# Performance work log

Measured on AMD Instinct MI355X. Metric: run time of the kernel, lower is better.

Reference implementation:

```python
import jax, jax.numpy as jnp
import numpy as np

IN_FEATURES = 4096
OUT_FEATURES = 11008
GROUPSIZE = 128
N_GROUPS = IN_FEATURES // GROUPSIZE  # 32


def setup_inputs() -> dict:
    key = jax.random.key(0)
    k1, k2, k3 = jax.random.split(key, 3)
    inp = jax.random.normal(k1, (2, 2048, IN_FEATURES), dtype=jnp.float32)
    # int8 quantized weights stored as int8
    weight = jax.random.randint(k2, (OUT_FEATURES, IN_FEATURES), -128, 128, dtype=jnp.int32).astype(jnp.int8)
    # per-(output-channel, group) positive scales
    scales = jax.random.uniform(k3, (OUT_FEATURES, N_GROUPS), dtype=jnp.float32) * 0.01 + 1e-4
    return {"input": inp, "weight": weight, "scales": scales}


def reference(input, weight, scales):
    # Dequantize: w[o, g, j] = int8_w[o, g, j] * scales[o, g]
    O, I = weight.shape
    w = weight.astype(input.dtype).reshape(O, N_GROUPS, GROUPSIZE)
    w = (w * scales[:, :, None].astype(input.dtype)).reshape(O, I)
    # F.linear: input @ w.T  -> [B, S, O]
    return jnp.einsum("bsi,oi->bso", input, w)
```

## Files before the change

kernel.cpp:

```cpp
#include <hip/hip_runtime.h>

#define MDIM 4096
#define KDIM 4096
#define NDIM 11008
#define NGROUPS 32

#define BM 256
#define BN 256
#define BK 64
#define NT (KDIM / BK)
#define KB (KDIM * 2)

typedef _Float16 f16x8 __attribute__((ext_vector_type(8)));
typedef float f32x4 __attribute__((ext_vector_type(4)));

typedef const unsigned int __attribute__((address_space(1))) *gas_t;
typedef unsigned int __attribute__((address_space(3))) *las_t;

__device__ __forceinline__ void gld_lds16(const void *g, void *l) {
  __builtin_amdgcn_global_load_lds((gas_t)g, (las_t)l, 16, 0, 0);
}

#define BAR() asm volatile("s_barrier" ::: "memory")
#define VMW4() asm volatile("s_waitcnt vmcnt(4)" ::: "memory")
#define VMW0() asm volatile("s_waitcnt vmcnt(0)" ::: "memory")
#define FENCE() __builtin_amdgcn_sched_barrier(0)

__global__ __launch_bounds__(256) void cvt_a_kernel(const float *__restrict__ a,
                                                    _Float16 *__restrict__ o) {
  const int n8 = (MDIM * KDIM) / 8;
  for (int i = blockIdx.x * blockDim.x + threadIdx.x; i < n8;
       i += gridDim.x * blockDim.x) {
    const float4 v0 = *(const float4 *)(a + (size_t)i * 8);
    const float4 v1 = *(const float4 *)(a + (size_t)i * 8 + 4);
    f16x8 h;
    h[0] = (_Float16)v0.x; h[1] = (_Float16)v0.y;
    h[2] = (_Float16)v0.z; h[3] = (_Float16)v0.w;
    h[4] = (_Float16)v1.x; h[5] = (_Float16)v1.y;
    h[6] = (_Float16)v1.z; h[7] = (_Float16)v1.w;
    *(f16x8 *)(o + (size_t)i * 8) = h;
  }
}

__global__ __launch_bounds__(256) void cvt_w_kernel(const int *__restrict__ w,
                                                    const float *__restrict__ s,
                                                    _Float16 *__restrict__ o) {
  const int n8 = (NDIM * KDIM) / 8;
  for (int i = blockIdx.x * blockDim.x + threadIdx.x; i < n8;
       i += gridDim.x * blockDim.x) {
    const size_t base = (size_t)i * 8;
    const int row = (int)(base >> 12);
    const int g = ((int)(base & (KDIM - 1))) >> 7;
    const float sc = s[row * NGROUPS + g];
    const int4 w0 = *(const int4 *)(w + base);
    const int4 w1 = *(const int4 *)(w + base + 4);
    f16x8 h;
    h[0] = (_Float16)((float)w0.x * sc); h[1] = (_Float16)((float)w0.y * sc);
    h[2] = (_Float16)((float)w0.z * sc); h[3] = (_Float16)((float)w0.w * sc);
    h[4] = (_Float16)((float)w1.x * sc); h[5] = (_Float16)((float)w1.y * sc);
    h[6] = (_Float16)((float)w1.z * sc); h[7] = (_Float16)((float)w1.w * sc);
    *(f16x8 *)(o + base) = h;
  }
}

__global__ __launch_bounds__(512, 2) void gemm_8phase(
    const _Float16 *__restrict__ Ah, const _Float16 *__restrict__ Wh,
    float *__restrict__ C) {
  __shared__ __align__(16) char Sh[163840];

  const int tid = threadIdx.x;
  const int l = tid & 63;
  const int w = tid >> 6;
  const int wm = w >> 2;
  const int wn = w & 3;

  const int wg = blockIdx.x;
  const int swz = (wg & 7) * 86 + (wg >> 3);
  const int bx = swz / 16;
  const int by = swz % 16;

  const int srow = l >> 3;
  const int gk = ((l & 7) ^ srow) * 16;
  const char *Ag =
      (const char *)Ah + (size_t)(by * BM + w * 8 + srow) * KB + gk;
  const char *Bg =
      (const char *)Wh + (size_t)(bx * BN + w * 8 + srow) * KB + gk;

  const int laneRow = (l & 15) * (BK * 2);
  const int kx0 = ((l >> 4) * 16) ^ ((l & 7) * 16);
  const int kx1 = kx0 ^ 64;

  f32x4 acc[8][4] = {};
  f16x8 af0[4][2], af1[4][2], bf0[2][2], bf1[2][2];

  unsigned aC = 0, aN = 32768;
  unsigned bC = 65536, bN = 98304, bS = 131072;

#define STAGE2_A(KT, OFF, S0)                                                 \
  {                                                                           \
    const char *ap_ = Ag + (size_t)(KT) * (BK * 2);                           \
    gld_lds16(ap_ + (size_t)(S0) * (64 * KB),                                 \
              (void *)(Sh + (OFF) + (S0) * 8192 + w * 1024));                 \
    gld_lds16(ap_ + (size_t)((S0) + 1) * (64 * KB),                           \
              (void *)(Sh + (OFF) + ((S0) + 1) * 8192 + w * 1024));           \
  }

#define STAGE2_B(KT, OFF, S0)                                                 \
  {                                                                           \
    const char *bp_ = Bg + (size_t)(KT) * (BK * 2);                           \
    gld_lds16(bp_ + (size_t)(S0) * (64 * KB),                                 \
              (void *)(Sh + (OFF) + (S0) * 8192 + w * 1024));                 \
    gld_lds16(bp_ + (size_t)((S0) + 1) * (64 * KB),                           \
              (void *)(Sh + (OFF) + ((S0) + 1) * 8192 + w * 1024));           \
  }

#define LDA_Q(DST, QM, BASE)                                                  \
  {                                                                           \
    const char *ba_ = (BASE) + (wm * 128 + (QM) * 64) * (BK * 2) + laneRow;   \
    _Pragma("unroll") for (int mi = 0; mi < 4; ++mi) {                        \
      DST[mi][0] = *(const f16x8 *)(ba_ + mi * 2048 + kx0);                   \
      DST[mi][1] = *(const f16x8 *)(ba_ + mi * 2048 + kx1);                   \
    }                                                                         \
  }

#define LDB_Q(DST, QN, BASE)                                                  \
  {                                                                           \
    const char *bb_ = (BASE) + (wn * 64 + (QN) * 32) * (BK * 2) + laneRow;    \
    _Pragma("unroll") for (int nj = 0; nj < 2; ++nj) {                        \
      DST[nj][0] = *(const f16x8 *)(bb_ + nj * 2048 + kx0);                   \
      DST[nj][1] = *(const f16x8 *)(bb_ + nj * 2048 + kx1);                   \
    }                                                                         \
  }

#define MMA_Q(AF, BF, QM, QN)                                                 \
  __builtin_amdgcn_s_setprio(1);                                              \
  _Pragma("unroll") for (int ks = 0; ks < 2; ++ks)                            \
      _Pragma("unroll") for (int mi = 0; mi < 4; ++mi)                        \
          _Pragma("unroll") for (int nj = 0; nj < 2; ++nj)                    \
              acc[(QM) * 4 + mi][(QN) * 2 + nj] =                             \
                  __builtin_amdgcn_mfma_f32_16x16x32_f16(                     \
                      AF[mi][ks], BF[nj][ks],                                 \
                      acc[(QM) * 4 + mi][(QN) * 2 + nj], 0, 0, 0);            \
  __builtin_amdgcn_s_setprio(0);

  STAGE2_A(0, aC, 0); STAGE2_A(0, aC, 2);
  STAGE2_B(0, bC, 0); STAGE2_B(0, bC, 2);
  STAGE2_B(1, bN, 0); STAGE2_B(1, bN, 2);
  VMW4();
  BAR();
  LDA_Q(af0, 0, (const char *)Sh + aC);
  LDB_Q(bf0, 0, (const char *)Sh + bC);

#pragma unroll 2
  for (int t = 0; t < NT; ++t) {
    const bool s1 = (t + 1 < NT);
    const bool s2 = (t + 2 < NT);
    const char *Ac = (const char *)Sh + aC;
    const char *An = (const char *)Sh + aN;
    const char *Bc = (const char *)Sh + bC;
    const char *Bn = (const char *)Sh + bN;

    if (s1) { STAGE2_A(t + 1, aN, 0); STAGE2_A(t + 1, aN, 2); }
    if (s2) { STAGE2_B(t + 2, bS, 0); STAGE2_B(t + 2, bS, 2); }

    LDB_Q(bf1, 1, Bc);
    FENCE();
    MMA_Q(af0, bf0, 0, 0);

    LDA_Q(af1, 1, Ac);
    FENCE();
    MMA_Q(af0, bf1, 0, 1);

    MMA_Q(af1, bf1, 1, 1);
    MMA_Q(af1, bf0, 1, 0);

    if (s2) { VMW4(); } else { VMW0(); }
    BAR();
    if (s1) {
      LDA_Q(af0, 0, An);
      LDB_Q(bf0, 0, Bn);
    }

    { const unsigned ta = aC; aC = aN; aN = ta; }
    { const unsigned tb = bC; bC = bN; bN = bS; bS = tb; }
  }

#undef STAGE2_A
#undef STAGE2_B
#undef LDA_Q
#undef LDB_Q
#undef MMA_Q

  const int fr = l & 15, fq = l >> 4;
  float *Cb = C + (size_t)(by * BM + wm * 128) * NDIM + bx * BN + wn * 64;
#pragma unroll
  for (int i = 0; i < 8; ++i)
#pragma unroll
    for (int j = 0; j < 4; ++j)
#pragma unroll
      for (int r = 0; r < 4; ++r)
        Cb[(size_t)(i * 16 + fq * 4 + r) * NDIM + j * 16 + fr] = acc[i][j][r];
}

__global__ __launch_bounds__(256) void gemm_fused(const float *__restrict__ A,
                                                  const int *__restrict__ W,
                                                  const float *__restrict__ S,
                                                  float *__restrict__ C) {
  __shared__ _Float16 Asf[128 * 64];
  __shared__ _Float16 Bsf[128 * 64];
  const int tid = threadIdx.x;
  const int lane = tid & 63;
  const int wv = tid >> 6;
  const int wm = wv >> 1, wn = wv & 1;
  const int bx = blockIdx.x, by = blockIdx.y;
  const int srow = tid >> 1;
  const int skof = (tid & 1) * 32;

  const float *Ab = A + (size_t)(by * 128 + srow) * KDIM + skof;
  const int *Wb = W + (size_t)(bx * 128 + srow) * KDIM + skof;
  const float *Sb = S + (size_t)(bx * 128 + srow) * NGROUPS;

  f32x4 acc[4][4] = {};
  float4 ar[8];
  int4 wr[8];
  float sc;

#pragma unroll
  for (int u = 0; u < 8; ++u) {
    ar[u] = *(const float4 *)(Ab + u * 4);
    wr[u] = *(const int4 *)(Wb + u * 4);
  }
  sc = Sb[0];

  const int fr = lane & 15;
  const int fq = lane >> 4;
  const int kbase = fq * 8;

  for (int kt = 0; kt < KDIM / 64; ++kt) {
    __syncthreads();
    _Float16 *Ad = &Asf[srow * 64 + skof];
    _Float16 *Bd = &Bsf[srow * 64 + skof];
#pragma unroll
    for (int u = 0; u < 4; ++u) {
      const float4 a0 = ar[2 * u], a1 = ar[2 * u + 1];
      const int4 b0 = wr[2 * u], b1 = wr[2 * u + 1];
      f16x8 ha, hb;
      ha[0] = (_Float16)a0.x; ha[1] = (_Float16)a0.y;
      ha[2] = (_Float16)a0.z; ha[3] = (_Float16)a0.w;
      ha[4] = (_Float16)a1.x; ha[5] = (_Float16)a1.y;
      ha[6] = (_Float16)a1.z; ha[7] = (_Float16)a1.w;
      hb[0] = (_Float16)((float)b0.x * sc); hb[1] = (_Float16)((float)b0.y * sc);
      hb[2] = (_Float16)((float)b0.z * sc); hb[3] = (_Float16)((float)b0.w * sc);
      hb[4] = (_Float16)((float)b1.x * sc); hb[5] = (_Float16)((float)b1.y * sc);
      hb[6] = (_Float16)((float)b1.z * sc); hb[7] = (_Float16)((float)b1.w * sc);
      *(f16x8 *)(Ad + u * 8) = ha;
      *(f16x8 *)(Bd + u * 8) = hb;
    }
    if (kt + 1 < KDIM / 64) {
      const float *An = Ab + (kt + 1) * 64;
      const int *Wn = Wb + (kt + 1) * 64;
#pragma unroll
      for (int u = 0; u < 8; ++u) {
        ar[u] = *(const float4 *)(An + u * 4);
        wr[u] = *(const int4 *)(Wn + u * 4);
      }
      sc = Sb[(kt + 1) >> 1];
    }
    __syncthreads();
#pragma unroll
    for (int ks = 0; ks < 2; ++ks) {
      f16x8 afv[4], bfv[4];
      const int kof = ks * 32 + kbase;
#pragma unroll
      for (int i = 0; i < 4; ++i) {
        afv[i] = *(const f16x8 *)&Asf[(wm * 64 + i * 16 + fr) * 64 + kof];
        bfv[i] = *(const f16x8 *)&Bsf[(wn * 64 + i * 16 + fr) * 64 + kof];
      }
#pragma unroll
      for (int i = 0; i < 4; ++i)
#pragma unroll
        for (int j = 0; j < 4; ++j)
          acc[i][j] = __builtin_amdgcn_mfma_f32_16x16x32_f16(afv[i], bfv[j],
                                                             acc[i][j], 0, 0, 0);
    }
  }

  float *Cb = C + (size_t)(by * 128 + wm * 64) * NDIM + bx * 128 + wn * 64;
#pragma unroll
  for (int i = 0; i < 4; ++i)
#pragma unroll
    for (int j = 0; j < 4; ++j)
#pragma unroll
      for (int r = 0; r < 4; ++r)
        Cb[(size_t)(i * 16 + fq * 4 + r) * NDIM + j * 16 + fr] = acc[i][j][r];
}

extern "C" void kernel_launch(void *const *d_in, const int *in_sizes, int n_in,
                              void *d_out, int out_size, void *d_ws,
                              size_t ws_size, hipStream_t stream) {
  (void)in_sizes; (void)n_in; (void)out_size;
  const float *A = (const float *)d_in[0];
  const int *W = (const int *)d_in[1];
  const float *S = (const float *)d_in[2];
  float *C = (float *)d_out;

  const size_t needA = (size_t)MDIM * KDIM * sizeof(_Float16);
  const size_t needW = (size_t)NDIM * KDIM * sizeof(_Float16);

  if (ws_size >= needA + needW) {
    _Float16 *Ahp = (_Float16 *)d_ws;
    _Float16 *Whp = (_Float16 *)((char *)d_ws + needA);
    cvt_a_kernel<<<2048, 256, 0, stream>>>(A, Ahp);
    cvt_w_kernel<<<2048, 256, 0, stream>>>(W, S, Whp);
    gemm_8phase<<<(MDIM / BM) * (NDIM / BN), 512, 0, stream>>>(Ahp, Whp, C);
  } else {
    dim3 grid(NDIM / 128, MDIM / 128);
    gemm_fused<<<grid, 256, 0, stream>>>(A, W, S, C);
  }
}
```

Baseline: 409.1 us.

## Interleave LDS fragment reads with MFMA chunks and ping-pong B registers

Splits the per-quarter LDS fragment loads and MFMA blocks into smaller pieces and interleaves them, so shared-memory reads are spread between MFMA groups. The last quarter's MFMAs now run after the barrier and overlap the loads of the next tile's A and B fragments. B fragment registers alternate between two buffers across a manually unrolled pair of tiles. The aim is to hide LDS latency and barrier stalls behind matrix work. The cost is more live registers, which may pressure occupancy, and heavier reliance on the compiler keeping the intended order across the fences.

```diff
diff --git a/kernel.cpp b/kernel.cpp
--- a/kernel.cpp
+++ b/kernel.cpp
@@ -91,7 +91,7 @@
   const int kx1 = kx0 ^ 64;
 
   f32x4 acc[8][4] = {};
-  f16x8 af0[4][2], af1[4][2], bf0[2][2], bf1[2][2];
+  f16x8 af0[4][2], af1[4][2], bfA[2][2], bfB[2][2];
 
   unsigned aC = 0, aN = 32768;
   unsigned bC = 65536, bN = 98304, bS = 131072;
@@ -114,81 +114,102 @@
               (void *)(Sh + (OFF) + ((S0) + 1) * 8192 + w * 1024));           \
   }
 
-#define LDA_Q(DST, QM, BASE)                                                  \
+#define RDA2(DST, MI, QM, BASE)                                               \
   {                                                                           \
     const char *ba_ = (BASE) + (wm * 128 + (QM) * 64) * (BK * 2) + laneRow;   \
-    _Pragma("unroll") for (int mi = 0; mi < 4; ++mi) {                        \
-      DST[mi][0] = *(const f16x8 *)(ba_ + mi * 2048 + kx0);                   \
-      DST[mi][1] = *(const f16x8 *)(ba_ + mi * 2048 + kx1);                   \
-    }                                                                         \
-  }
-
-#define LDB_Q(DST, QN, BASE)                                                  \
+    DST[MI][0] = *(const f16x8 *)(ba_ + (MI) * 2048 + kx0);                   \
+    DST[MI][1] = *(const f16x8 *)(ba_ + (MI) * 2048 + kx1);                   \
+  }
+
+#define RDB2(DST, NJ, QN, BASE)                                               \
   {                                                                           \
     const char *bb_ = (BASE) + (wn * 64 + (QN) * 32) * (BK * 2) + laneRow;    \
-    _Pragma("unroll") for (int nj = 0; nj < 2; ++nj) {                        \
-      DST[nj][0] = *(const f16x8 *)(bb_ + nj * 2048 + kx0);                   \
-      DST[nj][1] = *(const f16x8 *)(bb_ + nj * 2048 + kx1);                   \
-    }                                                                         \
-  }
+    DST[NJ][0] = *(const f16x8 *)(bb_ + (NJ) * 2048 + kx0);                   \
+    DST[NJ][1] = *(const f16x8 *)(bb_ + (NJ) * 2048 + kx1);                   \
+  }
+
+#define MMA4(AF, BF, QM, QN, KS, MI0)                                         \
+  __builtin_amdgcn_s_setprio(1);                                              \
+  _Pragma("unroll") for (int mi = (MI0); mi < (MI0) + 2; ++mi)                \
+      _Pragma("unroll") for (int nj = 0; nj < 2; ++nj)                        \
+          acc[(QM) * 4 + mi][(QN) * 2 + nj] =                                 \
+              __builtin_amdgcn_mfma_f32_16x16x32_f16(                         \
+                  AF[mi][KS], BF[nj][KS],                                     \
+                  acc[(QM) * 4 + mi][(QN) * 2 + nj], 0, 0, 0);                \
+  __builtin_amdgcn_s_setprio(0);
 
 #define MMA_Q(AF, BF, QM, QN)                                                 \
-  __builtin_amdgcn_s_setprio(1);                                              \
-  _Pragma("unroll") for (int ks = 0; ks < 2; ++ks)                            \
-      _Pragma("unroll") for (int mi = 0; mi < 4; ++mi)                        \
-          _Pragma("unroll") for (int nj = 0; nj < 2; ++nj)                    \
-              acc[(QM) * 4 + mi][(QN) * 2 + nj] =                             \
-                  __builtin_amdgcn_mfma_f32_16x16x32_f16(                     \
-                      AF[mi][ks], BF[nj][ks],                                 \
-                      acc[(QM) * 4 + mi][(QN) * 2 + nj], 0, 0, 0);            \
-  __builtin_amdgcn_s_setprio(0);
+  MMA4(AF, BF, QM, QN, 0, 0); MMA4(AF, BF, QM, QN, 0, 2);                     \
+  MMA4(AF, BF, QM, QN, 1, 0); MMA4(AF, BF, QM, QN, 1, 2);
+
+#define TILE(T, B0, B1)                                                       \
+  {                                                                           \
+    const bool s1 = (T) + 1 < NT;                                             \
+    const bool s2 = (T) + 2 < NT;                                             \
+    const char *Ac = (const char *)Sh + aC;                                   \
+    const char *An = (const char *)Sh + aN;                                   \
+    const char *Bc = (const char *)Sh + bC;                                   \
+    const char *Bn = (const char *)Sh + bN;                                   \
+       \
+    if (s1) { STAGE2_A((T) + 1, aN, 0); STAGE2_A((T) + 1, aN, 2); }           \
+    if (s2) { STAGE2_B((T) + 2, bS, 0); STAGE2_B((T) + 2, bS, 2); }           \
+                 \
+    RDB2(B1, 0, 1, Bc);                                                       \
+    FENCE(); MMA4(af0, B0, 0, 0, 0, 0);                                       \
+    RDB2(B1, 1, 1, Bc);                                                       \
+    FENCE(); MMA4(af0, B0, 0, 0, 0, 2);                                       \
+    FENCE(); MMA4(af0, B0, 0, 0, 1, 0);                                       \
+    FENCE(); MMA4(af0, B0, 0, 0, 1, 2);                                       \
+                \
+    RDA2(af1, 0, 1, Ac); RDA2(af1, 1, 1, Ac);                                 \
+    FENCE(); MMA4(af0, B1, 0, 1, 0, 0);                                       \
+    RDA2(af1, 2, 1, Ac); RDA2(af1, 3, 1, Ac);                                 \
+    FENCE(); MMA4(af0, B1, 0, 1, 0, 2);                                       \
+    FENCE(); MMA4(af0, B1, 0, 1, 1, 0);                                       \
+    FENCE(); MMA4(af0, B1, 0, 1, 1, 2);                                       \
+                                           \
+    MMA_Q(af1, B1, 1, 1);                                                     \
+              \
+    if (s2) { VMW4(); } else { VMW0(); }                                      \
+    BAR();                                                                    \
+             \
+    if (s1) { RDA2(af0, 0, 0, An); RDA2(af0, 1, 0, An); }                     \
+    FENCE(); MMA4(af1, B0, 1, 0, 0, 0);                                       \
+    if (s1) { RDA2(af0, 2, 0, An); RDA2(af0, 3, 0, An); }                     \
+    FENCE(); MMA4(af1, B0, 1, 0, 0, 2);                                       \
+    if (s1) { RDB2(B1, 0, 0, Bn); }                                           \
+    FENCE(); MMA4(af1, B0, 1, 0, 1, 0);                                       \
+    if (s1) { RDB2(B1, 1, 0, Bn); }                                           \
+    FENCE(); MMA4(af1, B0, 1, 0, 1, 2);                                       \
+                                                        \
+    { const unsigned ta = aC; aC = aN; aN = ta; }                             \
+    { const unsigned tb = bC; bC = bN; bN = bS; bS = tb; }                    \
+  }
 
   STAGE2_A(0, aC, 0); STAGE2_A(0, aC, 2);
   STAGE2_B(0, bC, 0); STAGE2_B(0, bC, 2);
   STAGE2_B(1, bN, 0); STAGE2_B(1, bN, 2);
   VMW4();
   BAR();
-  LDA_Q(af0, 0, (const char *)Sh + aC);
-  LDB_Q(bf0, 0, (const char *)Sh + bC);
-
-#pragma unroll 2
-  for (int t = 0; t < NT; ++t) {
-    const bool s1 = (t + 1 < NT);
-    const bool s2 = (t + 2 < NT);
-    const char *Ac = (const char *)Sh + aC;
-    const char *An = (const char *)Sh + aN;
-    const char *Bc = (const char *)Sh + bC;
-    const char *Bn = (const char *)Sh + bN;
-
-    if (s1) { STAGE2_A(t + 1, aN, 0); STAGE2_A(t + 1, aN, 2); }
-    if (s2) { STAGE2_B(t + 2, bS, 0); STAGE2_B(t + 2, bS, 2); }
-
-    LDB_Q(bf1, 1, Bc);
-    FENCE();
-    MMA_Q(af0, bf0, 0, 0);
-
-    LDA_Q(af1, 1, Ac);
-    FENCE();
-    MMA_Q(af0, bf1, 0, 1);
-
-    MMA_Q(af1, bf1, 1, 1);
-    MMA_Q(af1, bf0, 1, 0);
-
-    if (s2) { VMW4(); } else { VMW0(); }
-    BAR();
-    if (s1) {
-      LDA_Q(af0, 0, An);
-      LDB_Q(bf0, 0, Bn);
-    }
-
-    { const unsigned ta = aC; aC = aN; aN = ta; }
-    { const unsigned tb = bC; bC = bN; bN = bS; bS = tb; }
-  }
-
+  {
+    const char *A0 = (const char *)Sh + aC;
+    const char *B0p = (const char *)Sh + bC;
+    RDA2(af0, 0, 0, A0); RDA2(af0, 1, 0, A0);
+    RDA2(af0, 2, 0, A0); RDA2(af0, 3, 0, A0);
+    RDB2(bfA, 0, 0, B0p); RDB2(bfA, 1, 0, B0p);
+  }
+
+  for (int t = 0; t < NT; t += 2) {
+    TILE(t, bfA, bfB);
+    TILE(t + 1, bfB, bfA);
+  }
+
+#undef TILE
 #undef STAGE2_A
 #undef STAGE2_B
-#undef LDA_Q
-#undef LDB_Q
+#undef RDA2
+#undef RDB2
+#undef MMA4
 #undef MMA_Q
 
   const int fr = l & 15, fq = l >> 4;
```

Measured after the change: 398.2 us. 2.7% less time.

## Shrink GEMM tile to 128x128 and restructure the LDS pipeline for higher occupancy

Applied to the files above, without the earlier changes.

Reduces the block tile from 256x256 to 128x128 with 512 threads and halves shared memory so four workgroups can share a CU. The main loop is reworked to interleave per-fragment LDS reads with MFMA groups, and the next A tile is staged into the buffer just consumed instead of being prefetched up front. The workgroup swizzle is updated to match the larger grid. The aim is better latency hiding and less tail imbalance, at the cost of lower arithmetic intensity per tile and more global and LDS traffic per FLOP.

```diff
diff --git a/kernel.cpp b/kernel.cpp
--- a/kernel.cpp
+++ b/kernel.cpp
@@ -5,8 +5,8 @@
 #define NDIM 11008
 #define NGROUPS 32
 
-#define BM 256
-#define BN 256
+#define BM 128
+#define BN 128
 #define BK 64
 #define NT (KDIM / BK)
 #define KB (KDIM * 2)
@@ -23,6 +23,7 @@
 
 #define BAR() asm volatile("s_barrier" ::: "memory")
 #define VMW4() asm volatile("s_waitcnt vmcnt(4)" ::: "memory")
+#define VMW2() asm volatile("s_waitcnt vmcnt(2)" ::: "memory")
 #define VMW0() asm volatile("s_waitcnt vmcnt(0)" ::: "memory")
 #define FENCE() __builtin_amdgcn_sched_barrier(0)
 
@@ -63,10 +64,10 @@
   }
 }
 
-__global__ __launch_bounds__(512, 2) void gemm_8phase(
+__global__ __launch_bounds__(512, 4) void gemm_8phase(
     const _Float16 *__restrict__ Ah, const _Float16 *__restrict__ Wh,
     float *__restrict__ C) {
-  __shared__ __align__(16) char Sh[163840];
+  __shared__ __align__(16) char Sh[81920];
 
   const int tid = threadIdx.x;
   const int l = tid & 63;
@@ -75,9 +76,9 @@
   const int wn = w & 3;
 
   const int wg = blockIdx.x;
-  const int swz = (wg & 7) * 86 + (wg >> 3);
-  const int bx = swz / 16;
-  const int by = swz % 16;
+  const int swz = (wg & 7) * 344 + (wg >> 3);
+  const int bx = swz / 32;
+  const int by = swz % 32;
 
   const int srow = l >> 3;
   const int gk = ((l & 7) ^ srow) * 16;
@@ -86,72 +87,59 @@
   const char *Bg =
       (const char *)Wh + (size_t)(bx * BN + w * 8 + srow) * KB + gk;
 
-  const int laneRow = (l & 15) * (BK * 2);
+  const int laneRow = (l & 15) * 128;
   const int kx0 = ((l >> 4) * 16) ^ ((l & 7) * 16);
   const int kx1 = kx0 ^ 64;
 
-  f32x4 acc[8][4] = {};
-  f16x8 af0[4][2], af1[4][2], bf0[2][2], bf1[2][2];
-
-  unsigned aC = 0, aN = 32768;
-  unsigned bC = 65536, bN = 98304, bS = 131072;
-
-#define STAGE2_A(KT, OFF, S0)                                                 \
+  f32x4 acc[4][2] = {};
+  f16x8 af[4][2], bf[2][2];
+
+  unsigned aC = 0, aN = 16384;
+  unsigned bC = 32768, bN = 49152, bS = 65536;
+
+#define STAGE_A(KT, OFF)                                                      \
   {                                                                           \
     const char *ap_ = Ag + (size_t)(KT) * (BK * 2);                           \
-    gld_lds16(ap_ + (size_t)(S0) * (64 * KB),                                 \
-              (void *)(Sh + (OFF) + (S0) * 8192 + w * 1024));                 \
-    gld_lds16(ap_ + (size_t)((S0) + 1) * (64 * KB),                           \
-              (void *)(Sh + (OFF) + ((S0) + 1) * 8192 + w * 1024));           \
-  }
-
-#define STAGE2_B(KT, OFF, S0)                                                 \
+    gld_lds16(ap_, (void *)(Sh + (OFF) + w * 1024));                          \
+    gld_lds16(ap_ + (size_t)64 * KB, (void *)(Sh + (OFF) + 8192 + w * 1024)); \
+  }
+
+#define STAGE_B(KT, OFF)                                                      \
   {                                                                           \
     const char *bp_ = Bg + (size_t)(KT) * (BK * 2);                           \
-    gld_lds16(bp_ + (size_t)(S0) * (64 * KB),                                 \
-              (void *)(Sh + (OFF) + (S0) * 8192 + w * 1024));                 \
-    gld_lds16(bp_ + (size_t)((S0) + 1) * (64 * KB),                           \
-              (void *)(Sh + (OFF) + ((S0) + 1) * 8192 + w * 1024));           \
-  }
-
-#define LDA_Q(DST, QM, BASE)                                                  \
-  {                                                                           \
-    const char *ba_ = (BASE) + (wm * 128 + (QM) * 64) * (BK * 2) + laneRow;   \
-    _Pragma("unroll") for (int mi = 0; mi < 4; ++mi) {                        \
-      DST[mi][0] = *(const f16x8 *)(ba_ + mi * 2048 + kx0);                   \
-      DST[mi][1] = *(const f16x8 *)(ba_ + mi * 2048 + kx1);                   \
-    }                                                                         \
-  }
-
-#define LDB_Q(DST, QN, BASE)                                                  \
-  {                                                                           \
-    const char *bb_ = (BASE) + (wn * 64 + (QN) * 32) * (BK * 2) + laneRow;    \
-    _Pragma("unroll") for (int nj = 0; nj < 2; ++nj) {                        \
-      DST[nj][0] = *(const f16x8 *)(bb_ + nj * 2048 + kx0);                   \
-      DST[nj][1] = *(const f16x8 *)(bb_ + nj * 2048 + kx1);                   \
-    }                                                                         \
-  }
-
-#define MMA_Q(AF, BF, QM, QN)                                                 \
+    gld_lds16(bp_, (void *)(Sh + (OFF) + w * 1024));                          \
+    gld_lds16(bp_ + (size_t)64 * KB, (void *)(Sh + (OFF) + 8192 + w * 1024)); \
+  }
+
+#define RDA(MI, KS, BASE)                                                     \
+  af[MI][KS] = *(const f16x8 *)((BASE) + wm * 8192 + (MI) * 2048 + laneRow +  \
+                                ((KS) ? kx1 : kx0));
+
+#define RDB(NJ, KS, BASE)                                                     \
+  bf[NJ][KS] = *(const f16x8 *)((BASE) + wn * 4096 + (NJ) * 2048 + laneRow +  \
+                                ((KS) ? kx1 : kx0));
+
+#define MMA4(KS, MI0)                                                         \
   __builtin_amdgcn_s_setprio(1);                                              \
-  _Pragma("unroll") for (int ks = 0; ks < 2; ++ks)                            \
-      _Pragma("unroll") for (int mi = 0; mi < 4; ++mi)                        \
-          _Pragma("unroll") for (int nj = 0; nj < 2; ++nj)                    \
-              acc[(QM) * 4 + mi][(QN) * 2 + nj] =                             \
-                  __builtin_amdgcn_mfma_f32_16x16x32_f16(                     \
-                      AF[mi][ks], BF[nj][ks],                                 \
-                      acc[(QM) * 4 + mi][(QN) * 2 + nj], 0, 0, 0);            \
+  _Pragma("unroll") for (int mi = (MI0); mi < (MI0) + 2; ++mi)                \
+      _Pragma("unroll") for (int nj = 0; nj < 2; ++nj)                        \
+          acc[mi][nj] = __builtin_amdgcn_mfma_f32_16x16x32_f16(               \
+              af[mi][KS], bf[nj][KS], acc[mi][nj], 0, 0, 0);                  \
   __builtin_amdgcn_s_setprio(0);
 
-  STAGE2_A(0, aC, 0); STAGE2_A(0, aC, 2);
-  STAGE2_B(0, bC, 0); STAGE2_B(0, bC, 2);
-  STAGE2_B(1, bN, 0); STAGE2_B(1, bN, 2);
+  STAGE_A(0, aC);
+  STAGE_B(0, bC);
+  STAGE_B(1, bN);
+  STAGE_A(1, aN);
   VMW4();
   BAR();
-  LDA_Q(af0, 0, (const char *)Sh + aC);
-  LDB_Q(bf0, 0, (const char *)Sh + bC);
-
-#pragma unroll 2
+  {
+    const char *A0 = (const char *)Sh + aC;
+    const char *B0 = (const char *)Sh + bC;
+    RDA(0, 0, A0); RDA(1, 0, A0); RDA(2, 0, A0); RDA(3, 0, A0);
+    RDB(0, 0, B0); RDB(1, 0, B0);
+  }
+
   for (int t = 0; t < NT; ++t) {
     const bool s1 = (t + 1 < NT);
     const bool s2 = (t + 2 < NT);
@@ -160,43 +148,45 @@
     const char *Bc = (const char *)Sh + bC;
     const char *Bn = (const char *)Sh + bN;
 
-    if (s1) { STAGE2_A(t + 1, aN, 0); STAGE2_A(t + 1, aN, 2); }
-    if (s2) { STAGE2_B(t + 2, bS, 0); STAGE2_B(t + 2, bS, 2); }
-
-    LDB_Q(bf1, 1, Bc);
+    if (s2) { STAGE_B(t + 2, bS); }
+
+    RDB(0, 1, Bc);
+    RDB(1, 1, Bc);
+    FENCE(); MMA4(0, 0);
+
+    RDA(0, 1, Ac); RDA(1, 1, Ac);
+    FENCE(); MMA4(0, 2);
+    RDA(2, 1, Ac); RDA(3, 1, Ac);
     FENCE();
-    MMA_Q(af0, bf0, 0, 0);
-
-    LDA_Q(af1, 1, Ac);
+
+    if (s2) { VMW2(); } else { VMW0(); }
+    BAR();
+
+    if (s1) { RDA(0, 0, An); RDA(1, 0, An); }
+    FENCE(); MMA4(1, 0);
+    if (s1) { RDA(2, 0, An); RDA(3, 0, An); }
     FENCE();
-    MMA_Q(af0, bf1, 0, 1);
-
-    MMA_Q(af1, bf1, 1, 1);
-    MMA_Q(af1, bf0, 1, 0);
-
-    if (s2) { VMW4(); } else { VMW0(); }
-    BAR();
-    if (s1) {
-      LDA_Q(af0, 0, An);
-      LDB_Q(bf0, 0, Bn);
-    }
+
+    if (s1) { RDB(0, 0, Bn); RDB(1, 0, Bn); }
+    FENCE(); MMA4(1, 2);
+    if (s2) { STAGE_A(t + 2, aC); }
 
     { const unsigned ta = aC; aC = aN; aN = ta; }
     { const unsigned tb = bC; bC = bN; bN = bS; bS = tb; }
   }
 
-#undef STAGE2_A
-#undef STAGE2_B
-#undef LDA_Q
-#undef LDB_Q
-#undef MMA_Q
+#undef STAGE_A
+#undef STAGE_B
+#undef RDA
+#undef RDB
+#undef MMA4
 
   const int fr = l & 15, fq = l >> 4;
-  float *Cb = C + (size_t)(by * BM + wm * 128) * NDIM + bx * BN + wn * 64;
-#pragma unroll
-  for (int i = 0; i < 8; ++i)
-#pragma unroll
-    for (int j = 0; j < 4; ++j)
+  float *Cb = C + (size_t)(by * BM + wm * 64) * NDIM + bx * BN + wn * 32;
+#pragma unroll
+  for (int i = 0; i < 4; ++i)
+#pragma unroll
+    for (int j = 0; j < 2; ++j)
 #pragma unroll
       for (int r = 0; r < 4; ++r)
         Cb[(size_t)(i * 16 + fq * 4 + r) * NDIM + j * 16 + fr] = acc[i][j][r];
```

Result: slower. 496.5 us (+21.4%).
